# Optimization experiments

Hardware: AMD Instinct MI355X
Metric: run time of the kernel (lower is better)

## Reference

```python
import jax, jax.numpy as jnp
import numpy as np

B, F, O = 512, 4, 10          # batch, nFRAMES, objects per frame (last = destination)
H = W = 128                   # IMG_HEIGHT, IMG_WIDTH
BASE = H // 2                 # baseX = baseY = 64
OUT = 5                       # outDims (actions)


def _glorot(k, shape):
    fan_in = int(np.prod(shape[1:]))
    return (jax.random.normal(k, shape, jnp.float32) / np.sqrt(fan_in)).astype(jnp.float32)


def setup_inputs() -> dict:
    key = jax.random.key(0)
    ks = jax.random.split(key, 11)
    x = jax.random.randint(ks[0], (B, F, O, 2), -30, 31, dtype=jnp.int32)
    return {
        "x": x,
        "w1": _glorot(ks[1], (32, F, 7, 7)), "b1": jnp.zeros((32,), jnp.float32),
        "w2": _glorot(ks[2], (64, 32, 5, 5)), "b2": jnp.zeros((64,), jnp.float32),
        "w3": _glorot(ks[3], (128, 64, 3, 3)), "b3": jnp.zeros((128,), jnp.float32),
        "fw1": _glorot(ks[4], (128, 128)), "fb1": jnp.zeros((128,), jnp.float32),
        "fw2": _glorot(ks[5], (OUT, 128)), "fb2": jnp.zeros((OUT,), jnp.float32),
    }


def rasterize(x):
    """Vectorized equivalent of the python-loop fill/fillPath rasterization.
    x: [B, F, O, 2] int32. Returns t: [B, F, H, W] float32."""
    xi = x.astype(jnp.int32)
    d = xi[:, :, -1, :]                       # destination per (batch, frame)
    dX = BASE + d[..., 0]                     # [B,F]
    dY = BASE - d[..., 1]                     # [B,F] (intended d[1]; original b[1] is a bug)
    xs = jnp.arange(W)
    ys = jnp.arange(H)
    # X-phase of fillPath: marks (baseY, x) for x from baseX toward dX, excluding dX
    loX = jnp.where(dX >= BASE, BASE, dX + 1)
    hiX = jnp.where(dX >= BASE, dX - 1, BASE)
    maskX = (xs >= loX[..., None]) & (xs <= hiX[..., None])          # [B,F,W]
    # Y-phase: marks (y, dX) for y from baseY toward dY, excluding dY
    loY = jnp.where(dY >= BASE, BASE, dY + 1)
    hiY = jnp.where(dY >= BASE, dY - 1, BASE)
    maskY = (ys >= loY[..., None]) & (ys <= hiY[..., None])          # [B,F,H]
    rowhot = (ys == BASE)                                            # [H]
    colhot = (xs[None, None, None, :] == dX[..., None, None])        # [B,F,1,W]
    path = (maskX[:, :, None, :] & rowhot[None, None, :, None]) | (maskY[:, :, :, None] & colhot)
    t = jnp.where(path, jnp.float32(-1.0), jnp.float32(0.0))         # [B,F,H,W]
    # base marker (fill at baseX, baseY): 3x3 ring of 0.5, center 1.0 (overwrites path)
    t = t.at[:, :, BASE - 1:BASE + 2, BASE - 1:BASE + 2].set(0.5)
    t = t.at[:, :, BASE, BASE].set(1.0)
    # object markers, in original sequential order (later objects overwrite earlier)
    bi = jnp.arange(B)[:, None, None, None]
    fi = jnp.arange(F)[None, :, None, None]
    offs = jnp.arange(-1, 2)
    dn = offs[:, None]
    dm = offs[None, :]
    for k in range(O - 1):
        a = (xi[:, :, k, 0] + BASE) % (W - 1)     # [B,F] column center
        b = (BASE - xi[:, :, k, 1]) % (H - 1)     # [B,F] row center
        iy = b[:, :, None, None] + dn             # [B,F,3,3]; -1 wraps like torch
        ix = a[:, :, None, None] + dm
        t = t.at[bi, fi, iy, ix].set(0.5)
        t = t.at[jnp.arange(B)[:, None], jnp.arange(F)[None, :], b, a].set(1.0)
    return t


def _conv(x, w, b, stride, pad):
    y = jax.lax.conv_general_dilated(x, w, (stride, stride), [(pad, pad), (pad, pad)],
                                     dimension_numbers=('NCHW', 'OIHW', 'NCHW'))
    return y + b[None, :, None, None]


def _maxpool(x, k, s):
    return jax.lax.reduce_window(x, -jnp.inf, jax.lax.max, (1, 1, k, k), (1, 1, s, s), 'VALID')


def net(t, w1, b1, w2, b2, w3, b3, fw1, fb1, fw2, fb2):
    h = _maxpool(jax.nn.relu(_conv(t, w1, b1, 2, 3)), 3, 2)   # [B,32,31,31]
    h = _maxpool(jax.nn.relu(_conv(h, w2, b2, 1, 2)), 2, 2)   # [B,64,15,15]
    h = _maxpool(jax.nn.relu(_conv(h, w3, b3, 1, 1)), 2, 2)   # [B,128,7,7]
    h = jnp.mean(h, axis=(2, 3))                               # AdaptiveAvgPool2d(1) + Flatten
    h = jax.nn.relu(h @ fw1.T + fb1)
    return h @ fw2.T + fb2                                     # [B, OUT]


def reference(x, w1, b1, w2, b2, w3, b3, fw1, fb1, fw2, fb2):
    t = rasterize(x)
    return net(t, w1, b1, w2, b2, w3, b3, fw1, fb1, fw2, fb2)
```

## Files before the change

kernel.cpp:

```cpp
#include <hip/hip_runtime.h>
#include <cstddef>

typedef unsigned short ushort_t;
typedef unsigned uv4 __attribute__((ext_vector_type(4)));
typedef unsigned uv2 __attribute__((ext_vector_type(2)));
typedef float f32x4 __attribute__((ext_vector_type(4)));

constexpr int Bfull = 512;
constexpr int F = 4, O = 10;

constexpr size_t TB_B  = (size_t)136 * 136 * 4 * 2;
constexpr size_t C1_B  = (size_t)64 * 64 * 32 * 4;
constexpr size_t P1_B  = (size_t)35 * 35 * 32 * 2;
constexpr size_t P2_B  = (size_t)17 * 18 * 64 * 2;
constexpr size_t FEAT_B = (size_t)Bfull * 128 * 4;
constexpr size_t W1P_ELEMS = (size_t)7 * 4 * 16 * 32;
constexpr size_t W2P_ELEMS = (size_t)25 * 2 * 64 * 32;
constexpr size_t W3P_ELEMS = (size_t)9 * 2 * 2 * 128 * 32;

__device__ __forceinline__ ushort_t f2bf_rne(float x) {
    unsigned u = __builtin_bit_cast(unsigned, x);
    unsigned r = (u + 0x7FFFu + ((u >> 16) & 1u)) >> 16;
    return (ushort_t)r;
}
__device__ __forceinline__ float bf2f(ushort_t b) {
    return __builtin_bit_cast(float, (unsigned)b << 16);
}

#define MFMA16(acc, a, b) \
    asm("v_mfma_f32_16x16x32_bf16 %0, %1, %2, %0" : "+v"(acc) : "v"(a), "v"(b))

__global__ __launch_bounds__(256) void rasterize_bf_k(const int* __restrict__ x,
                                                      ushort_t* __restrict__ tb, int b0) {
    int b_l = blockIdx.x;
    int rg  = blockIdx.y;
    int b = b0 + b_l;
    __shared__ int pts[F][O][2];
    __shared__ int prm[F][24];
    int tid = threadIdx.x;
    if (tid < F * O * 2)
        ((int*)pts)[tid] = x[(size_t)b * F * O * 2 + tid];
    __syncthreads();
    if (tid < F) {
        int f = tid;
        int dX = 64 + pts[f][O - 1][0];
        int dY = 64 - pts[f][O - 1][1];
        prm[f][0] = dX; prm[f][1] = dY;
        prm[f][2] = dX >= 64 ? 64 : dX + 1; prm[f][3] = dX >= 64 ? dX - 1 : 64;
        prm[f][4] = dY >= 64 ? 64 : dY + 1; prm[f][5] = dY >= 64 ? dY - 1 : 64;
        for (int k = 0; k < O - 1; ++k) {
            prm[f][6 + k]  = (pts[f][k][0] + 64) % 127;
            prm[f][15 + k] = (64 - pts[f][k][1]) % 127;
        }
    }
    __syncthreads();
    ushort_t* outp = tb + (size_t)b_l * 136 * 136 * 4;
    int r0 = rg * 17;
    for (int i = tid; i < 17 * 136; i += 256) {
        int r = r0 + i / 136, c = i % 136;
        int y = r - 3, xx = c - 3;
        unsigned pack0 = 0, pack1 = 0;
        if (y >= 0 && y < 128 && xx >= 0 && xx < 128) {
            bool ctr9 = (y >= 63 && y <= 65 && xx >= 63 && xx <= 65);
            bool ctr1 = (y == 64 && xx == 64);
            #pragma unroll
            for (int f = 0; f < 4; ++f) {
                unsigned bf;
                if (ctr1) bf = 0x3F80u;
                else if (ctr9) bf = 0x3F00u;
                else {
                    int dX = prm[f][0];
                    bool mX = (xx >= prm[f][2]) && (xx <= prm[f][3]);
                    bool mY = (y >= prm[f][4]) && (y <= prm[f][5]);
                    bf = ((mX && y == 64) || (mY && xx == dX)) ? 0xBF80u : 0u;
                }
                if (f & 1) { if (f >> 1) pack1 |= bf << 16; else pack0 |= bf << 16; }
                else       { if (f >> 1) pack1 |= bf;       else pack0 |= bf; }
            }
        }
        uv2 pk; pk.x = pack0; pk.y = pack1;
        *(uv2*)(outp + ((size_t)r * 136 + c) * 4) = pk;
    }
    __syncthreads();
    if (tid < 4) {
        int f = tid;
        int r1 = r0 + 17;
        for (int k = 0; k < O - 1; ++k) {
            int a = prm[f][6 + k] + 3, bb = prm[f][15 + k] + 3;
            #pragma unroll
            for (int dy = -1; dy <= 1; ++dy) {
                int rr = bb + dy;
                if (rr >= r0 && rr < r1) {
                    ushort_t* rowp = outp + ((size_t)rr * 136 + a - 1) * 4 + f;
                    rowp[0] = 0x3F00u; rowp[4] = 0x3F00u; rowp[8] = 0x3F00u;
                }
            }
            if (bb >= r0 && bb < r1) outp[((size_t)bb * 136 + a) * 4 + f] = 0x3F80u;
        }
    }
}

__global__ __launch_bounds__(256) void prep_w1_k(const float* __restrict__ w1,
                                                 ushort_t* __restrict__ w1p) {
    int idx = blockIdx.x * 256 + threadIdx.x;
    if (idx >= (int)W1P_ELEMS) return;
    int k = idx & 31, lr = (idx >> 5) & 15, slot = (idx >> 9) & 3, ky = idx >> 11;
    int hl = slot & 1, m = slot >> 1;
    int kx = k >> 2, ic = k & 3;
    int oc = m * 16 + lr;
    float w = (kx < 7) ? w1[((oc * 4 + ic) * 7 + ky) * 7 + kx] : 0.f;
    ushort_t h = f2bf_rne(w);
    w1p[idx] = hl ? f2bf_rne(w - bf2f(h)) : h;
}

__global__ __launch_bounds__(256) void conv1_mfma_k(const ushort_t* __restrict__ tb,
                                                    const ushort_t* __restrict__ w1p,
                                                    const float* __restrict__ b1,
                                                    unsigned* __restrict__ c1p) {
    int b_l = blockIdx.x;
    int oyt = blockIdx.y;
    int wave = threadIdx.x >> 6, lane = threadIdx.x & 63;
    int lr = lane & 15, lq = lane >> 4;
    const ushort_t* tbb = tb + (size_t)b_l * 136 * 136 * 4;
    int aoff = lr * 32 + lq * 8;
    float bias[2][4];
    #pragma unroll
    for (int m = 0; m < 2; ++m)
        #pragma unroll
        for (int j = 0; j < 4; ++j)
            bias[m][j] = b1[m * 16 + lq * 4 + j];
    int oybase = oyt * 16 + wave * 4;
    #pragma unroll 1
    for (int yy = 0; yy < 4; ++yy) {
        int oy = oybase + yy;
        f32x4 acc[2][4];
        #pragma unroll
        for (int m = 0; m < 2; ++m)
            #pragma unroll
            for (int xt = 0; xt < 4; ++xt)
                acc[m][xt] = (f32x4)0.f;
        #pragma unroll
        for (int ky = 0; ky < 7; ++ky) {
            const ushort_t* wb = w1p + (size_t)ky * 2048;
            uv4 ah0 = *(const uv4*)(wb + aoff);
            uv4 al0 = *(const uv4*)(wb + 512 + aoff);
            uv4 ah1 = *(const uv4*)(wb + 1024 + aoff);
            uv4 al1 = *(const uv4*)(wb + 1536 + aoff);
            const ushort_t* rb = tbb + (size_t)(2 * oy + ky) * (136 * 4);
            #pragma unroll
            for (int xt = 0; xt < 4; ++xt) {
                uv4 bv = *(const uv4*)(rb + (size_t)(2 * (xt * 16 + lr) + 2 * lq) * 4);
                MFMA16(acc[0][xt], ah0, bv);
                MFMA16(acc[1][xt], ah1, bv);
                MFMA16(acc[0][xt], al0, bv);
                MFMA16(acc[1][xt], al1, bv);
            }
        }
        asm volatile("s_nop 7\n\ts_nop 7");
        #pragma unroll
        for (int m = 0; m < 2; ++m)
            #pragma unroll
            for (int xt = 0; xt < 4; ++xt) {
                uv4 pk;
                #pragma unroll
                for (int j = 0; j < 4; ++j) {
                    float v = fmaxf(acc[m][xt][j] + bias[m][j], 0.f);
                    ushort_t h = f2bf_rne(v);
                    ushort_t l = f2bf_rne(v - bf2f(h));
                    pk[j] = (unsigned)h | ((unsigned)l << 16);
                }
                *(uv4*)(c1p + (((size_t)b_l * 64 + oy) * 64 + xt * 16 + lr) * 32 + m * 16 + lq * 4) = pk;
            }
    }
}

__global__ __launch_bounds__(256) void pool1b_k(const unsigned* __restrict__ c1p,
                                                ushort_t* __restrict__ p1h,
                                                ushort_t* __restrict__ p1l, int n) {
    int idx = blockIdx.x * 256 + threadIdx.x;
    if (idx >= n) return;
    int ic = idx & 31; int t = idx >> 5;
    int pc = t % 35; t /= 35;
    int pr = t % 35; int b = t / 35;
    int py = pr - 2, px = pc - 2;
    float v = 0.f;
    if (py >= 0 && py < 31 && px >= 0 && px < 31) {
        const unsigned* base = c1p + (((size_t)b * 64 + 2 * py) * 64 + 2 * px) * 32 + ic;
        #pragma unroll
        for (int r = 0; r < 3; ++r)
            #pragma unroll
            for (int c = 0; c < 3; ++c) {
                unsigned u = base[(r * 64 + c) * 32];
                float f = bf2f((ushort_t)(u & 0xFFFFu)) + bf2f((ushort_t)(u >> 16));
                v = fmaxf(v, f);
            }
    }
    ushort_t h = f2bf_rne(v);
    p1h[idx] = h;
    p1l[idx] = f2bf_rne(v - bf2f(h));
}

__global__ __launch_bounds__(256) void prep_w2_k(const float* __restrict__ w2,
                                                 ushort_t* __restrict__ w2p) {
    int idx = blockIdx.x * 256 + threadIdx.x;
    if (idx >= 25 * 64 * 32) return;
    int ic = idx & 31, oc = (idx >> 5) & 63, kk = idx >> 11;
    float w = w2[(size_t)(oc * 32 + ic) * 25 + kk];
    ushort_t h = f2bf_rne(w);
    w2p[(size_t)kk * 4096 + (idx & 2047)] = h;
    w2p[(size_t)kk * 4096 + 2048 + (idx & 2047)] = f2bf_rne(w - bf2f(h));
}

__global__ __launch_bounds__(256) void zero_pad_k(ushort_t* __restrict__ p2h,
                                                  ushort_t* __restrict__ p2l, int n) {
    int idx = blockIdx.x * 256 + threadIdx.x;
    if (idx >= n) return;
    int ic = idx & 63; int t = idx >> 6;
    int cell = t % 81; int t2 = t / 81;
    int pl = t2 & 1; int b = t2 >> 1;
    int r, c;
    if (cell < 18) { r = 0; c = cell; }
    else if (cell < 36) { r = 16; c = cell - 18; }
    else { int q = cell - 36; r = 1 + q / 3; int m = q % 3; c = (m == 0) ? 0 : 15 + m; }
    size_t off = (((size_t)b * 17 + r) * 18 + c) * 64 + ic;
    (pl ? p2l : p2h)[off] = 0;
}

__global__ __launch_bounds__(256) void conv2_mfma_k(const ushort_t* __restrict__ p1h,
                                                    const ushort_t* __restrict__ p1l,
                                                    const ushort_t* __restrict__ w2p,
                                                    const float* __restrict__ b2,
                                                    ushort_t* __restrict__ p2h,
                                                    ushort_t* __restrict__ p2l) {
    __shared__ ushort_t sB[2][13440];
    int b_l = blockIdx.x;
    int yt  = blockIdx.y;
    int y0 = yt * 8;
    int nrows = (35 - y0) < 12 ? (35 - y0) : 12;
    int tid = threadIdx.x;

    {
        int nchunks = nrows * 35 * 4;
        const ushort_t* src0 = p1h + (size_t)b_l * 35 * 1120 + (size_t)y0 * 1120;
        const ushort_t* src1 = p1l + (size_t)b_l * 35 * 1120 + (size_t)y0 * 1120;
        for (int c = tid; c < 2 * nchunks; c += 256) {
            int p = c >= nchunks;
            int cc = p ? c - nchunks : c;
            int lqi = cc & 3;
            int pc = (cc >> 2) % 35;
            int r = cc / 140;
            const ushort_t* s = p ? src1 : src0;
            uv4 v = *(const uv4*)(s + (size_t)r * 1120 + pc * 32 + lqi * 8);
            int swz = lqi ^ ((pc >> 1) & 3);
            *(uv4*)(&sB[p][(r * 35 + pc) * 32 + swz * 8]) = v;
        }
    }
    __syncthreads();

    int wave = threadIdx.x >> 6;
    int lane = threadIdx.x & 63;
    int wm = wave & 1, wy = wave >> 1;
    int oc0 = wm * 32;
    int lr = lane & 15, lq = lane >> 4;
    int rclip = 34 - y0;

    f32x4 acc[4][2][2];
    #pragma unroll
    for (int y = 0; y < 4; ++y)
        #pragma unroll
        for (int m = 0; m < 2; ++m)
            #pragma unroll
            for (int n = 0; n < 2; ++n)
                acc[y][m][n] = (f32x4)0.f;

    int aoff = (oc0 + lr) * 32 + lq * 8;

    #pragma unroll 1
    for (int kk = 0; kk < 25; ++kk) {
        int ky = kk / 5, kx = kk % 5;
        const ushort_t* wb = w2p + (size_t)kk * 4096;
        uv4 ah0 = *(const uv4*)(wb + aoff);
        uv4 ah1 = *(const uv4*)(wb + aoff + 512);
        uv4 al0 = *(const uv4*)(wb + 2048 + aoff);
        uv4 al1 = *(const uv4*)(wb + 2048 + aoff + 512);
        int pcc[2];
        #pragma unroll
        for (int xt = 0; xt < 2; ++xt) {
            int pc = xt * 16 + lr + kx; pc = pc > 34 ? 34 : pc;
            pcc[xt] = pc * 32 + (lq ^ ((pc >> 1) & 3)) * 8;
        }
        #pragma unroll
        for (int y = 0; y < 4; ++y) {
            int r = wy * 4 + y + ky; r = r > rclip ? rclip : r;
            int rbase = r * 1120;
            #pragma unroll
            for (int xt = 0; xt < 2; ++xt) {
                int off = rbase + pcc[xt];
                uv4 bh = *(const uv4*)(&sB[0][off]);
                uv4 bl = *(const uv4*)(&sB[1][off]);
                MFMA16(acc[y][0][xt], ah0, bh);
                MFMA16(acc[y][1][xt], ah1, bh);
                MFMA16(acc[y][0][xt], ah0, bl);
                MFMA16(acc[y][1][xt], ah1, bl);
                MFMA16(acc[y][0][xt], al0, bh);
                MFMA16(acc[y][1][xt], al1, bh);
            }
        }
    }
    asm volatile("s_nop 7\n\ts_nop 7");

    float bias[2][4];
    #pragma unroll
    for (int m = 0; m < 2; ++m)
        #pragma unroll
        for (int j = 0; j < 4; ++j)
            bias[m][j] = b2[oc0 + m * 16 + lq * 4 + j];

    int ybase = y0 + wy * 4;
    #pragma unroll
    for (int yp = 0; yp < 2; ++yp) {
        int yy = ybase + 2 * yp;
        if (yy + 1 > 30) continue;
        int py = yy >> 1;
        #pragma unroll
        for (int m = 0; m < 2; ++m)
            #pragma unroll
            for (int xt = 0; xt < 2; ++xt)
                #pragma unroll
                for (int j = 0; j < 4; ++j) {
                    float v = fmaxf(acc[2 * yp][m][xt][j], acc[2 * yp + 1][m][xt][j]);
                    float o = __shfl_xor(v, 1, 64);
                    v = fmaxf(fmaxf(v, o) + bias[m][j], 0.f);
                    int px = xt * 8 + (lr >> 1);
                    if (!(lane & 1) && px < 15) {
                        int oc = oc0 + m * 16 + lq * 4 + j;
                        size_t oo = (((size_t)b_l * 17 + py + 1) * 18 + px + 1) * 64 + oc;
                        ushort_t h = f2bf_rne(v);
                        p2h[oo] = h;
                        p2l[oo] = f2bf_rne(v - bf2f(h));
                    }
                }
    }
}

__global__ __launch_bounds__(256) void prep_w3_k(const float* __restrict__ w3,
                                                 ushort_t* __restrict__ w3p) {
    int idx = blockIdx.x * 256 + threadIdx.x;
    if (idx >= (int)W3P_ELEMS) return;
    int kk = idx & 31, oc = (idx >> 5) & 127, hl = (idx >> 12) & 1, ks = (idx >> 13) & 1, kxy = idx >> 14;
    int ky = kxy / 3, kx = kxy % 3;
    int ic = ks * 32 + kk;
    float w = w3[((size_t)(oc * 64 + ic) * 3 + ky) * 3 + kx];
    ushort_t h = f2bf_rne(w);
    w3p[idx] = hl ? f2bf_rne(w - bf2f(h)) : h;
}

__global__ __launch_bounds__(256) void conv3pool_k(const ushort_t* __restrict__ p2h,
                                                   const ushort_t* __restrict__ p2l,
                                                   const ushort_t* __restrict__ w3p,
                                                   const float* __restrict__ b3,
                                                   float* __restrict__ feat, int b0) {
    __shared__ ushort_t sB[2][19584];
    int b_l = blockIdx.x;
    int tid = threadIdx.x;
    {
        const ushort_t* s0 = p2h + (size_t)b_l * 19584;
        const ushort_t* s1 = p2l + (size_t)b_l * 19584;
        for (int ccg = tid; ccg < 4896; ccg += 256) {
            int p = ccg >= 2448;
            int cc = p ? ccg - 2448 : ccg;
            int rc = cc >> 3, slot = cc & 7;
            int c = rc % 18;
            uv4 v = *(const uv4*)((p ? s1 : s0) + (size_t)cc * 8);
            *(uv4*)(&sB[p][rc * 64 + (slot ^ (c & 7)) * 8]) = v;
        }
    }
    __syncthreads();
    int wave = tid >> 6, lane = tid & 63;
    int lr = lane & 15, lq = lane >> 4;
    int oc0 = wave * 32;
    float bias[2][4];
    #pragma unroll
    for (int m = 0; m < 2; ++m)
        #pragma unroll
        for (int j = 0; j < 4; ++j)
            bias[m][j] = b3[oc0 + m * 16 + lq * 4 + j];
    f32x4 fsum[2];
    fsum[0] = (f32x4)0.f; fsum[1] = (f32x4)0.f;

    int cl = lr;
    #pragma unroll 1
    for (int pr = 0; pr < 7; ++pr) {
        f32x4 acc[2][2];
        #pragma unroll
        for (int rr = 0; rr < 2; ++rr) { acc[rr][0] = (f32x4)0.f; acc[rr][1] = (f32x4)0.f; }
        #pragma unroll 1
        for (int ky = 0; ky < 3; ++ky)
            #pragma unroll 1
            for (int kx = 0; kx < 3; ++kx) {
                int c = cl + kx;
                int cs = c & 7;
                #pragma unroll
                for (int ks = 0; ks < 2; ++ks) {
                    const ushort_t* wb = w3p + (size_t)(((ky * 3 + kx) * 2 + ks) * 2) * 4096;
                    uv4 ah0 = *(const uv4*)(wb + (oc0 + lr) * 32 + lq * 8);
                    uv4 ah1 = *(const uv4*)(wb + (oc0 + 16 + lr) * 32 + lq * 8);
                    uv4 al0 = *(const uv4*)(wb + 4096 + (oc0 + lr) * 32 + lq * 8);
                    uv4 al1 = *(const uv4*)(wb + 4096 + (oc0 + 16 + lr) * 32 + lq * 8);
                    int slotk = ((ks << 2) | lq) ^ cs;
                    #pragma unroll
                    for (int rr = 0; rr < 2; ++rr) {
                        int r = 2 * pr + rr + ky;
                        int off = (r * 18 + c) * 64 + slotk * 8;
                        uv4 bh = *(const uv4*)(&sB[0][off]);
                        uv4 bl = *(const uv4*)(&sB[1][off]);
                        MFMA16(acc[rr][0], ah0, bh);
                        MFMA16(acc[rr][1], ah1, bh);
                        MFMA16(acc[rr][0], ah0, bl);
                        MFMA16(acc[rr][1], ah1, bl);
                        MFMA16(acc[rr][0], al0, bh);
                        MFMA16(acc[rr][1], al1, bh);
                    }
                }
            }
        asm volatile("s_nop 7\n\ts_nop 7");
        #pragma unroll
        for (int m = 0; m < 2; ++m)
            #pragma unroll
            for (int j = 0; j < 4; ++j) {
                float v0 = fmaxf(acc[0][m][j] + bias[m][j], 0.f);
                float v1 = fmaxf(acc[1][m][j] + bias[m][j], 0.f);
                float vm = fmaxf(v0, v1);
                float o = __shfl_xor(vm, 1, 64);
                float pooled = fmaxf(vm, o);
                if (lr < 14) fsum[m][j] += pooled;
            }
    }
    #pragma unroll
    for (int m = 0; m < 2; ++m)
        #pragma unroll
        for (int j = 0; j < 4; ++j) {
            float t = fsum[m][j];
            t += __shfl_xor(t, 1, 64);
            t += __shfl_xor(t, 2, 64);
            t += __shfl_xor(t, 4, 64);
            t += __shfl_xor(t, 8, 64);
            if (lr == 0)
                feat[(size_t)(b0 + b_l) * 128 + oc0 + m * 16 + lq * 4 + j] = t * (1.f / 98.f);
        }
}

__global__ __launch_bounds__(128) void fc_k(const float* __restrict__ feat,
                                            const float* __restrict__ fw1,
                                            const float* __restrict__ fb1,
                                            const float* __restrict__ fw2,
                                            const float* __restrict__ fb2,
                                            float* __restrict__ out) {
    __shared__ float sF[128];
    __shared__ float sH[128];
    int b = blockIdx.x, tid = threadIdx.x;
    sF[tid] = feat[(size_t)b * 128 + tid];
    __syncthreads();
    const float4* wrow = (const float4*)(fw1 + (size_t)tid * 128);
    float s = fb1[tid];
    #pragma unroll
    for (int i = 0; i < 32; ++i) {
        float4 w = wrow[i];
        s = fmaf(w.x, sF[4 * i], s);
        s = fmaf(w.y, sF[4 * i + 1], s);
        s = fmaf(w.z, sF[4 * i + 2], s);
        s = fmaf(w.w, sF[4 * i + 3], s);
    }
    sH[tid] = fmaxf(s, 0.f);
    __syncthreads();
    if (tid < 5) {
        const float* w2r = fw2 + (size_t)tid * 128;
        float s2 = fb2[tid];
        for (int i = 0; i < 128; ++i) s2 = fmaf(w2r[i], sH[i], s2);
        out[(size_t)b * 5 + tid] = s2;
    }
}

extern "C" void kernel_launch(void* const* d_in, const int* in_sizes, int n_in,
                              void* d_out, int out_size, void* d_ws, size_t ws_size,
                              hipStream_t stream) {
    const int*   x   = (const int*)d_in[0];
    const float* w1  = (const float*)d_in[1];
    const float* b1  = (const float*)d_in[2];
    const float* w2  = (const float*)d_in[3];
    const float* b2  = (const float*)d_in[4];
    const float* w3  = (const float*)d_in[5];
    const float* b3  = (const float*)d_in[6];
    const float* fw1 = (const float*)d_in[7];
    const float* fb1 = (const float*)d_in[8];
    const float* fw2 = (const float*)d_in[9];
    const float* fb2 = (const float*)d_in[10];
    float* out = (float*)d_out;

    const size_t per_img = C1_B + TB_B + 2 * P1_B + 2 * P2_B;
    const size_t fixed_b = FEAT_B + (W1P_ELEMS + W2P_ELEMS + W3P_ELEMS) * 2 + 1024;
    int NB = Bfull;
    while (NB > 128 && fixed_b + per_img * (size_t)NB > ws_size) NB >>= 1;

    char* base = (char*)d_ws;
    unsigned* c1p = (unsigned*)base;                    base += (size_t)NB * C1_B;
    float* feat = (float*)base;                         base += FEAT_B;
    ushort_t* tb  = (ushort_t*)base;                    base += (size_t)NB * TB_B;
    ushort_t* p1h = (ushort_t*)base;                    base += (size_t)NB * P1_B;
    ushort_t* p1l = (ushort_t*)base;                    base += (size_t)NB * P1_B;
    ushort_t* p2h = (ushort_t*)base;                    base += (size_t)NB * P2_B;
    ushort_t* p2l = (ushort_t*)base;                    base += (size_t)NB * P2_B;
    ushort_t* w1p = (ushort_t*)base;                    base += W1P_ELEMS * 2;
    ushort_t* w2p = (ushort_t*)base;                    base += W2P_ELEMS * 2;
    ushort_t* w3p = (ushort_t*)base;

    prep_w1_k<<<((int)W1P_ELEMS + 255) / 256, 256, 0, stream>>>(w1, w1p);
    prep_w2_k<<<(25 * 64 * 32 + 255) / 256, 256, 0, stream>>>(w2, w2p);
    prep_w3_k<<<((int)W3P_ELEMS + 255) / 256, 256, 0, stream>>>(w3, w3p);

    const int nchunk = Bfull / NB;
    const int pad_n = NB * 81 * 64 * 2;
    const int p1_n = NB * 35 * 35 * 32;
    for (int ch = 0; ch < nchunk; ++ch) {
        int b0 = ch * NB;
        rasterize_bf_k<<<dim3(NB, 8), 256, 0, stream>>>(x, tb, b0);
        conv1_mfma_k<<<dim3(NB, 4), 256, 0, stream>>>(tb, w1p, b1, c1p);
        pool1b_k<<<(p1_n + 255) / 256, 256, 0, stream>>>(c1p, p1h, p1l, p1_n);
        zero_pad_k<<<(pad_n + 255) / 256, 256, 0, stream>>>(p2h, p2l, pad_n);
        conv2_mfma_k<<<dim3(NB, 4), 256, 0, stream>>>(p1h, p1l, w2p, b2, p2h, p2l);
        conv3pool_k<<<NB, 256, 0, stream>>>(p2h, p2l, w3p, b3, feat, b0);
    }
    fc_k<<<Bfull, 128, 0, stream>>>(feat, fw1, fb1, fw2, fb2, out);
}
```

Baseline: 481.1 us.

## Fuse maxpool1 into conv1 epilogue and replace padding kernel with load-time masking

Conv1 now keeps its post-ReLU output in registers, does the vertical 3-row max across overlapping row groups (computing 5 conv rows per wave instead of 4), then stages partial maxima in shared memory for the horizontal pass. It writes pooled hi/lo bf16 values straight to p1, which removes the large c1p intermediate and the separate pool kernel. The zero-padding kernel is also dropped: conv2 and conv3 now zero border cells when loading into shared memory instead of relying on pre-zeroed buffers. The cost is redundant conv1 row computation (overlapping rows), a large shared-memory tile that may lower occupancy, and extra predicate logic in the loaders.

```diff
diff --git a/kernel.cpp b/kernel.cpp
--- a/kernel.cpp
+++ b/kernel.cpp
@@ -10,7 +10,6 @@
 constexpr int F = 4, O = 10;
 
 constexpr size_t TB_B  = (size_t)136 * 136 * 4 * 2;
-constexpr size_t C1_B  = (size_t)64 * 64 * 32 * 4;
 constexpr size_t P1_B  = (size_t)35 * 35 * 32 * 2;
 constexpr size_t P2_B  = (size_t)17 * 18 * 64 * 2;
 constexpr size_t FEAT_B = (size_t)Bfull * 128 * 4;
@@ -113,12 +112,14 @@
     w1p[idx] = hl ? f2bf_rne(w - bf2f(h)) : h;
 }
 
-__global__ __launch_bounds__(256) void conv1_mfma_k(const ushort_t* __restrict__ tb,
-                                                    const ushort_t* __restrict__ w1p,
-                                                    const float* __restrict__ b1,
-                                                    unsigned* __restrict__ c1p) {
+__global__ __launch_bounds__(256) void conv1pool_k(const ushort_t* __restrict__ tb,
+                                                   const ushort_t* __restrict__ w1p,
+                                                   const float* __restrict__ b1,
+                                                   ushort_t* __restrict__ p1h,
+                                                   ushort_t* __restrict__ p1l) {
+    __shared__ float sP[8 * 64 * 33];
     int b_l = blockIdx.x;
-    int oyt = blockIdx.y;
+    int yt  = blockIdx.y;
     int wave = threadIdx.x >> 6, lane = threadIdx.x & 63;
     int lr = lane & 15, lq = lane >> 4;
     const ushort_t* tbb = tb + (size_t)b_l * 136 * 136 * 4;
@@ -129,10 +130,20 @@
         #pragma unroll
         for (int j = 0; j < 4; ++j)
             bias[m][j] = b1[m * 16 + lq * 4 + j];
-    int oybase = oyt * 16 + wave * 4;
+    int base = yt * 16 + wave * 4;
+
+    f32x4 pacc[2][2][4];
+    #pragma unroll
+    for (int p = 0; p < 2; ++p)
+        #pragma unroll
+        for (int m = 0; m < 2; ++m)
+            #pragma unroll
+            for (int xt = 0; xt < 4; ++xt)
+                pacc[p][m][xt] = (f32x4)0.f;
+
     #pragma unroll 1
-    for (int yy = 0; yy < 4; ++yy) {
-        int oy = oybase + yy;
+    for (int rr = 0; rr < 5; ++rr) {
+        int oy = base + rr; oy = oy > 63 ? 63 : oy;
         f32x4 acc[2][4];
         #pragma unroll
         for (int m = 0; m < 2; ++m)
@@ -160,44 +171,41 @@
         #pragma unroll
         for (int m = 0; m < 2; ++m)
             #pragma unroll
-            for (int xt = 0; xt < 4; ++xt) {
-                uv4 pk;
+            for (int xt = 0; xt < 4; ++xt)
                 #pragma unroll
                 for (int j = 0; j < 4; ++j) {
                     float v = fmaxf(acc[m][xt][j] + bias[m][j], 0.f);
-                    ushort_t h = f2bf_rne(v);
-                    ushort_t l = f2bf_rne(v - bf2f(h));
-                    pk[j] = (unsigned)h | ((unsigned)l << 16);
+                    if (rr <= 2) pacc[0][m][xt][j] = fmaxf(pacc[0][m][xt][j], v);
+                    if (rr >= 2) pacc[1][m][xt][j] = fmaxf(pacc[1][m][xt][j], v);
                 }
-                *(uv4*)(c1p + (((size_t)b_l * 64 + oy) * 64 + xt * 16 + lr) * 32 + m * 16 + lq * 4) = pk;
-            }
-    }
-}
-
-__global__ __launch_bounds__(256) void pool1b_k(const unsigned* __restrict__ c1p,
-                                                ushort_t* __restrict__ p1h,
-                                                ushort_t* __restrict__ p1l, int n) {
-    int idx = blockIdx.x * 256 + threadIdx.x;
-    if (idx >= n) return;
-    int ic = idx & 31; int t = idx >> 5;
-    int pc = t % 35; t /= 35;
-    int pr = t % 35; int b = t / 35;
-    int py = pr - 2, px = pc - 2;
-    float v = 0.f;
-    if (py >= 0 && py < 31 && px >= 0 && px < 31) {
-        const unsigned* base = c1p + (((size_t)b * 64 + 2 * py) * 64 + 2 * px) * 32 + ic;
-        #pragma unroll
-        for (int r = 0; r < 3; ++r)
-            #pragma unroll
-            for (int c = 0; c < 3; ++c) {
-                unsigned u = base[(r * 64 + c) * 32];
-                float f = bf2f((ushort_t)(u & 0xFFFFu)) + bf2f((ushort_t)(u >> 16));
-                v = fmaxf(v, f);
-            }
-    }
-    ushort_t h = f2bf_rne(v);
-    p1h[idx] = h;
-    p1l[idx] = f2bf_rne(v - bf2f(h));
+    }
+
+    int prow0 = 2 * wave;
+    #pragma unroll
+    for (int pr = 0; pr < 2; ++pr)
+        #pragma unroll
+        for (int m = 0; m < 2; ++m)
+            #pragma unroll
+            for (int xt = 0; xt < 4; ++xt) {
+                int col = xt * 16 + lr;
+                float* dst = &sP[((prow0 + pr) * 64 + col) * 33 + m * 16 + lq * 4];
+                #pragma unroll
+                for (int j = 0; j < 4; ++j) dst[j] = pacc[pr][m][xt][j];
+            }
+    __syncthreads();
+
+    for (int i = threadIdx.x; i < 8 * 31 * 32; i += 256) {
+        int ch = i & 31; int t = i >> 5;
+        int px = t % 31; int r = t / 31;
+        int py = yt * 8 + r;
+        if (py > 30) continue;
+        const float* s = &sP[((size_t)r * 64 + 2 * px) * 33 + ch];
+        float v = fmaxf(fmaxf(s[0], s[33]), s[66]);
+        ushort_t h = f2bf_rne(v);
+        size_t addr = (((size_t)b_l * 35 + py + 2) * 35 + px + 2) * 32 + ch;
+        p1h[addr] = h;
+        p1l[addr] = f2bf_rne(v - bf2f(h));
+    }
 }
 
 __global__ __launch_bounds__(256) void prep_w2_k(const float* __restrict__ w2,
@@ -209,21 +217,6 @@
     ushort_t h = f2bf_rne(w);
     w2p[(size_t)kk * 4096 + (idx & 2047)] = h;
     w2p[(size_t)kk * 4096 + 2048 + (idx & 2047)] = f2bf_rne(w - bf2f(h));
-}
-
-__global__ __launch_bounds__(256) void zero_pad_k(ushort_t* __restrict__ p2h,
-                                                  ushort_t* __restrict__ p2l, int n) {
-    int idx = blockIdx.x * 256 + threadIdx.x;
-    if (idx >= n) return;
-    int ic = idx & 63; int t = idx >> 6;
-    int cell = t % 81; int t2 = t / 81;
-    int pl = t2 & 1; int b = t2 >> 1;
-    int r, c;
-    if (cell < 18) { r = 0; c = cell; }
-    else if (cell < 36) { r = 16; c = cell - 18; }
-    else { int q = cell - 36; r = 1 + q / 3; int m = q % 3; c = (m == 0) ? 0 : 15 + m; }
-    size_t off = (((size_t)b * 17 + r) * 18 + c) * 64 + ic;
-    (pl ? p2l : p2h)[off] = 0;
 }
 
 __global__ __launch_bounds__(256) void conv2_mfma_k(const ushort_t* __restrict__ p1h,
@@ -249,8 +242,11 @@
             int lqi = cc & 3;
             int pc = (cc >> 2) % 35;
             int r = cc / 140;
+            int pr_g = y0 + r;
+            bool inb = (pr_g >= 2 && pr_g <= 32 && pc >= 2 && pc <= 32);
             const ushort_t* s = p ? src1 : src0;
             uv4 v = *(const uv4*)(s + (size_t)r * 1120 + pc * 32 + lqi * 8);
+            if (!inb) v = (uv4)0u;
             int swz = lqi ^ ((pc >> 1) & 3);
             *(uv4*)(&sB[p][(r * 35 + pc) * 32 + swz * 8]) = v;
         }
@@ -370,8 +366,10 @@
             int p = ccg >= 2448;
             int cc = p ? ccg - 2448 : ccg;
             int rc = cc >> 3, slot = cc & 7;
-            int c = rc % 18;
+            int r = rc / 18, c = rc % 18;
+            bool pad = (r == 0 || r == 16 || c == 0 || c >= 16);
             uv4 v = *(const uv4*)((p ? s1 : s0) + (size_t)cc * 8);
+            if (pad) v = (uv4)0u;
             *(uv4*)(&sB[p][rc * 64 + (slot ^ (c & 7)) * 8]) = v;
         }
     }
@@ -497,13 +495,12 @@
     const float* fb2 = (const float*)d_in[10];
     float* out = (float*)d_out;
 
-    const size_t per_img = C1_B + TB_B + 2 * P1_B + 2 * P2_B;
+    const size_t per_img = TB_B + 2 * P1_B + 2 * P2_B;
     const size_t fixed_b = FEAT_B + (W1P_ELEMS + W2P_ELEMS + W3P_ELEMS) * 2 + 1024;
     int NB = Bfull;
     while (NB > 128 && fixed_b + per_img * (size_t)NB > ws_size) NB >>= 1;
 
     char* base = (char*)d_ws;
-    unsigned* c1p = (unsigned*)base;                    base += (size_t)NB * C1_B;
     float* feat = (float*)base;                         base += FEAT_B;
     ushort_t* tb  = (ushort_t*)base;                    base += (size_t)NB * TB_B;
     ushort_t* p1h = (ushort_t*)base;                    base += (size_t)NB * P1_B;
@@ -519,14 +516,10 @@
     prep_w3_k<<<((int)W3P_ELEMS + 255) / 256, 256, 0, stream>>>(w3, w3p);
 
     const int nchunk = Bfull / NB;
-    const int pad_n = NB * 81 * 64 * 2;
-    const int p1_n = NB * 35 * 35 * 32;
     for (int ch = 0; ch < nchunk; ++ch) {
         int b0 = ch * NB;
         rasterize_bf_k<<<dim3(NB, 8), 256, 0, stream>>>(x, tb, b0);
-        conv1_mfma_k<<<dim3(NB, 4), 256, 0, stream>>>(tb, w1p, b1, c1p);
-        pool1b_k<<<(p1_n + 255) / 256, 256, 0, stream>>>(c1p, p1h, p1l, p1_n);
-        zero_pad_k<<<(pad_n + 255) / 256, 256, 0, stream>>>(p2h, p2l, pad_n);
+        conv1pool_k<<<dim3(NB, 4), 256, 0, stream>>>(tb, w1p, b1, p1h, p1l);
         conv2_mfma_k<<<dim3(NB, 4), 256, 0, stream>>>(p1h, p1l, w2p, b2, p2h, p2l);
         conv3pool_k<<<NB, 256, 0, stream>>>(p2h, p2l, w3p, b3, feat, b0);
     }
```

New measurement: 446.4 us. -7.2%, faster.
